# Kernel tuning notes

Hardware: AMD Instinct MI355X
Metric: run time of the kernel (lower is better)

The kernel has to match this reference:

```python
import jax, jax.numpy as jnp
import numpy as np

B, L, D = 4, 2048, 256
MAX_NGRAM = 3
SLOTS = 64


def setup_inputs() -> dict:
    key = jax.random.key(0)
    k1, k2, k3 = jax.random.split(key, 3)
    x = jax.random.normal(k1, (B, L, D), dtype=jnp.float32)
    memory = jax.random.normal(k2, (SLOTS, MAX_NGRAM, D), dtype=jnp.float32)
    pos_bias = jax.random.normal(k3, (SLOTS, MAX_NGRAM), dtype=jnp.float32)
    return {"x": x, "memory": memory, "pos_bias": pos_bias}


def _extract_ngrams(x, max_ngram):
    # Left-pad with max_ngram-1 zero vectors, then take max_ngram shifted views.
    b, l, d = x.shape
    xpad = jnp.concatenate([jnp.zeros((b, max_ngram - 1, d), x.dtype), x], axis=1)
    # ngrams[b, l, n] = xpad[b, n + l]  -> (B, L, N, d)
    return jnp.stack([xpad[:, n:n + l] for n in range(max_ngram)], axis=2)


def reference(x, memory, pos_bias):
    slots, max_ngram, d = memory.shape
    ngrams = _extract_ngrams(x, max_ngram)                      # (B, L, N, d)
    # Contraction over d replaces the huge (B,L,M,N,d) broadcast-multiply.
    sims = jnp.einsum('blnd,mnd->blmn', ngrams, memory)         # (B, L, M, N)
    scores = sims + pos_bias[None, None]                        # (B, L, M, N)
    best = jnp.argmax(scores, axis=-1)                          # (B, L, M) int
    # selected[b,l,m] = memory[m, best[b,l,m]]  -> (B, L, M, d)
    selected = memory[jnp.arange(slots)[None, None, :], best]
    return selected.sum(axis=2)                                 # (B, L, d)
```

## Files before the change

### kernel.cpp

```cpp
#include <hip/hip_runtime.h>
#include <stdint.h>

#define LL   2048
#define DD   256
#define SLOTS 64
#define MN   192
#define PT   8192

typedef _Float16 half8 __attribute__((ext_vector_type(8)));
typedef float    f32x4 __attribute__((ext_vector_type(4)));

#define FRAG_ELEMS (MN * DD)

__global__ __launch_bounds__(256) void prep_kernel(
    const float* __restrict__ mem,
    _Float16* __restrict__ aS_h, _Float16* __restrict__ aS_l,
    _Float16* __restrict__ bG_h)
{
    const int e = blockIdx.x * 256 + threadIdx.x;
    const int mnp = e >> 8;
    const int d   = e & 255;
    const int n = mnp >> 6, m = mnp & 63;
    const float v = mem[((m * 3 + n) << 8) + d];
    const _Float16 h  = (_Float16)v;
    const _Float16 lo = (_Float16)(v - (float)h);

    {
        const int tm = mnp >> 4, r = mnp & 15;
        const int c = d >> 5, q = (d >> 3) & 3, j = d & 7;
        const int i1 = ((tm * 8 + c) * 64 + (q * 16 + r)) * 8 + j;
        aS_h[i1] = h; aS_l[i1] = lo;
    }
    {
        const int c2 = mnp >> 5, q2 = (mnp >> 3) & 3, j2 = mnp & 7;
        const int td = d >> 4, n2 = d & 15;
        const int i2 = ((td * 6 + c2) * 64 + (q2 * 16 + n2)) * 8 + j2;
        bG_h[i2] = h;
    }
}

__global__ __launch_bounds__(768, 3) void fused_kernel(
    const float* __restrict__ x, const float* __restrict__ bias,
    const _Float16* __restrict__ aS_h, const _Float16* __restrict__ aS_l,
    const _Float16* __restrict__ bG_h,
    float* __restrict__ out)
{
    __shared__ __align__(16) _Float16 xfh[3 * 8 * 64 * 8];
    __shared__ __align__(16) _Float16 xfl[3 * 8 * 64 * 8];
    __shared__ float    scores[MN * 35];
    __shared__ float    biasS[MN];
    __shared__ uint32_t selS[32 * 8];

    const int p0   = blockIdx.x * 32;
    const int tid  = threadIdx.x;
    const int lane = tid & 63;
    const int w    = tid >> 6;
    const int q    = lane >> 4, col = lane & 15;
    const int tm   = w;

    half8 ah[2], al[2];
    {
        const size_t off = (size_t)((tm * 8 + 0) * 64 + lane) * 8;
        ah[0] = *(const half8*)(aS_h + off);
        al[0] = *(const half8*)(aS_l + off);
    }

    if (tid < MN) {
        const int m = tid & 63, n = tid >> 6;
        biasS[tid] = bias[m * 3 + n];
    }

#pragma unroll
    for (int k = 0; k < 2; ++k) {
        const int idx = tid + k * 768;
        const int rr  = idx >> 5;
        const int ch  = idx & 31;
        int g = p0 - 2 + rr;
        g = g < 0 ? 0 : (g > PT - 1 ? PT - 1 : g);
        const float4* xr = (const float4*)(x + (size_t)g * DD + ch * 8);
        const float4 u = xr[0];
        const float4 v = xr[1];
        float f[8] = {u.x, u.y, u.z, u.w, v.x, v.y, v.z, v.w};
        half8 hi, lo;
#pragma unroll
        for (int j = 0; j < 8; ++j) {
            const _Float16 hh = (_Float16)f[j];
            hi[j] = hh;
            lo[j] = (_Float16)(f[j] - (float)hh);
        }
        const int c = ch >> 2, qq = ch & 3;
        const int pt = rr >> 4, lr = rr & 15;
        const int base = ((pt * 8 + c) * 64 + qq * 16 + lr) * 8;
        *(half8*)(xfh + base) = hi;
        *(half8*)(xfl + base) = lo;
    }
    __syncthreads();

    {
        f32x4 acc[3];
#pragma unroll
        for (int p = 0; p < 3; ++p) acc[p] = (f32x4){0.f, 0.f, 0.f, 0.f};

        half8 bh[2][3], bl[2][3];
#pragma unroll
        for (int p = 0; p < 3; ++p) {
            const int base = ((p * 8 + 0) * 64 + lane) * 8;
            bh[0][p] = *(const half8*)(xfh + base);
            bl[0][p] = *(const half8*)(xfl + base);
        }

#pragma unroll
        for (int c = 0; c < 8; ++c) {
            const int cur = c & 1, nxt = cur ^ 1;
            if (c < 7) {
                const size_t off = (size_t)((tm * 8 + c + 1) * 64 + lane) * 8;
                ah[nxt] = *(const half8*)(aS_h + off);
                al[nxt] = *(const half8*)(aS_l + off);
#pragma unroll
                for (int p = 0; p < 3; ++p) {
                    const int base = ((p * 8 + c + 1) * 64 + lane) * 8;
                    bh[nxt][p] = *(const half8*)(xfh + base);
                    bl[nxt][p] = *(const half8*)(xfl + base);
                }
            }
#pragma unroll
            for (int p = 0; p < 3; ++p) {
                acc[p] = __builtin_amdgcn_mfma_f32_16x16x32_f16(ah[cur], bh[cur][p], acc[p], 0, 0, 0);
                acc[p] = __builtin_amdgcn_mfma_f32_16x16x32_f16(ah[cur], bl[cur][p], acc[p], 0, 0, 0);
                acc[p] = __builtin_amdgcn_mfma_f32_16x16x32_f16(al[cur], bh[cur][p], acc[p], 0, 0, 0);
            }
        }

#pragma unroll
        for (int p = 0; p < 3; ++p) {
            const int wp = p * 16 + col;
            if (wp < 34) {
#pragma unroll
                for (int r = 0; r < 4; ++r)
                    scores[(tm * 16 + q * 4 + r) * 35 + wp] = acc[p][r];
            }
        }
    }

    half8 mg[2];
    mg[0] = *(const half8*)(bG_h + (size_t)((w * 6 + 0) * 64 + lane) * 8);
    __syncthreads();

    for (int pl = w; pl < 32; pl += 12) {
        const int m = lane;
        const int p = p0 + pl;
        const int l = p & (LL - 1);
        const float v0 = ((l >= 2) ? scores[(      m) * 35 + pl + 0] : 0.f) + biasS[      m];
        const float v1 = ((l >= 1) ? scores[( 64 + m) * 35 + pl + 1] : 0.f) + biasS[ 64 + m];
        const float v2 =             scores[(128 + m) * 35 + pl + 2]        + biasS[128 + m];
        int bn = 0; float bv = v0;
        if (v1 > bv) { bv = v1; bn = 1; }
        if (v2 > bv) { bv = v2; bn = 2; }
        const unsigned long long b0 = __ballot(bn == 0);
        const unsigned long long b1 = __ballot(bn == 1);
        const unsigned long long b2 = __ballot(bn == 2);
        if (lane < 6) {
            const unsigned long long B = (lane >> 1) == 0 ? b0 : ((lane >> 1) == 1 ? b1 : b2);
            selS[pl * 8 + lane] = (uint32_t)(B >> ((lane & 1) * 32));
        }
    }
    __syncthreads();

    {
        const _Float16 ONE = (_Float16)1.f, ZERO = (_Float16)0.f;
        const int qb = q * 8;
#pragma unroll
        for (int ti = 0; ti < 3; ++ti) {
            const int t = w + ti * 12;
            if (t < 32) {
                const int pt = t >> 4, td = t & 15;
                uint32_t sw[6];
#pragma unroll
                for (int c = 0; c < 6; ++c) sw[c] = selS[(pt * 16 + col) * 8 + c];

                f32x4 acc2 = (f32x4){0.f, 0.f, 0.f, 0.f};
#pragma unroll
                for (int c = 0; c < 6; ++c) {
                    const int cur = c & 1, nxt = cur ^ 1;
                    if (c < 5) {
                        mg[nxt] = *(const half8*)(bG_h + (size_t)((td * 6 + c + 1) * 64 + lane) * 8);
                    } else {
                        const int tn = t + 12;
                        if (tn < 32) {
                            const int tdn = tn & 15;
                            mg[nxt] = *(const half8*)(bG_h + (size_t)((tdn * 6 + 0) * 64 + lane) * 8);
                        }
                    }
                    half8 sel;
#pragma unroll
                    for (int j = 0; j < 8; ++j)
                        sel[j] = ((sw[c] >> (qb + j)) & 1u) ? ONE : ZERO;
                    acc2 = __builtin_amdgcn_mfma_f32_16x16x32_f16(sel, mg[cur], acc2, 0, 0, 0);
                }

#pragma unroll
                for (int r = 0; r < 4; ++r)
                    out[(size_t)(p0 + pt * 16 + q * 4 + r) * DD + td * 16 + col] = acc2[r];
            }
        }
    }
}

extern "C" void kernel_launch(void* const* d_in, const int* in_sizes, int n_in,
                              void* d_out, int out_size, void* d_ws, size_t ws_size,
                              hipStream_t stream) {
    (void)in_sizes; (void)n_in; (void)out_size; (void)ws_size;
    const float* x    = (const float*)d_in[0];
    const float* mem  = (const float*)d_in[1];
    const float* bias = (const float*)d_in[2];
    float* out = (float*)d_out;

    _Float16* aS_h = (_Float16*)d_ws;
    _Float16* aS_l = aS_h + FRAG_ELEMS;
    _Float16* bG_h = aS_l + FRAG_ELEMS;

    prep_kernel<<<FRAG_ELEMS / 256, 256, 0, stream>>>(mem, aS_h, aS_l, bG_h);
    fused_kernel<<<PT / 32, 768, 0, stream>>>(x, bias, aS_h, aS_l, bG_h, out);
}
```

Measured before the change: 73.32 us.

## Fuse memory fp16 split prep into main kernel and stage gather operand in LDS

Removes the separate prep kernel. Each block now reads the fp32 memory table directly, splits it into hi/lo fp16 MFMA A-fragments held in registers, and writes the hi-only gather operand into shared memory. The x staging buffer is aliased with the score buffer to keep LDS usage in check. This drops one kernel launch and the workspace round trip, at the cost of every block redundantly converting the whole memory table, plus higher register and LDS pressure.

```diff
diff --git a/kernel.cpp b/kernel.cpp
--- a/kernel.cpp
+++ b/kernel.cpp
@@ -10,46 +10,19 @@
 typedef _Float16 half8 __attribute__((ext_vector_type(8)));
 typedef float    f32x4 __attribute__((ext_vector_type(4)));
 
-#define FRAG_ELEMS (MN * DD)
-
-__global__ __launch_bounds__(256) void prep_kernel(
-    const float* __restrict__ mem,
-    _Float16* __restrict__ aS_h, _Float16* __restrict__ aS_l,
-    _Float16* __restrict__ bG_h)
-{
-    const int e = blockIdx.x * 256 + threadIdx.x;
-    const int mnp = e >> 8;
-    const int d   = e & 255;
-    const int n = mnp >> 6, m = mnp & 63;
-    const float v = mem[((m * 3 + n) << 8) + d];
-    const _Float16 h  = (_Float16)v;
-    const _Float16 lo = (_Float16)(v - (float)h);
-
-    {
-        const int tm = mnp >> 4, r = mnp & 15;
-        const int c = d >> 5, q = (d >> 3) & 3, j = d & 7;
-        const int i1 = ((tm * 8 + c) * 64 + (q * 16 + r)) * 8 + j;
-        aS_h[i1] = h; aS_l[i1] = lo;
-    }
-    {
-        const int c2 = mnp >> 5, q2 = (mnp >> 3) & 3, j2 = mnp & 7;
-        const int td = d >> 4, n2 = d & 15;
-        const int i2 = ((td * 6 + c2) * 64 + (q2 * 16 + n2)) * 8 + j2;
-        bG_h[i2] = h;
-    }
-}
-
 __global__ __launch_bounds__(768, 3) void fused_kernel(
-    const float* __restrict__ x, const float* __restrict__ bias,
-    const _Float16* __restrict__ aS_h, const _Float16* __restrict__ aS_l,
-    const _Float16* __restrict__ bG_h,
+    const float* __restrict__ x, const float* __restrict__ mem,
+    const float* __restrict__ bias,
     float* __restrict__ out)
 {
-    __shared__ __align__(16) _Float16 xfh[3 * 8 * 64 * 8];
-    __shared__ __align__(16) _Float16 xfl[3 * 8 * 64 * 8];
-    __shared__ float    scores[MN * 35];
+    __shared__ __align__(16) char xbuf[49152];
+    __shared__ __align__(16) _Float16 bGs[16 * 6 * 64 * 8];
     __shared__ float    biasS[MN];
-    __shared__ uint32_t selS[32 * 8];
+    __shared__ uint32_t selS[32 * 6];
+
+    _Float16* xfh = (_Float16*)xbuf;
+    _Float16* xfl = (_Float16*)(xbuf + 24576);
+    float*    scores = (float*)xbuf;
 
     const int p0   = blockIdx.x * 32;
     const int tid  = threadIdx.x;
@@ -58,21 +31,28 @@
     const int q    = lane >> 4, col = lane & 15;
     const int tm   = w;
 
-    half8 ah[2], al[2];
-    {
-        const size_t off = (size_t)((tm * 8 + 0) * 64 + lane) * 8;
-        ah[0] = *(const half8*)(aS_h + off);
-        al[0] = *(const half8*)(aS_l + off);
-    }
-
     if (tid < MN) {
         const int m = tid & 63, n = tid >> 6;
         biasS[tid] = bias[m * 3 + n];
     }
 
-#pragma unroll
-    for (int k = 0; k < 2; ++k) {
-        const int idx = tid + k * 768;
+    float gv[8][8];
+#pragma unroll
+    for (int k = 0; k < 8; ++k) {
+        const int combo = w + k * 12;
+        const int td = combo / 6, c2 = combo - td * 6;
+        const int q2 = lane >> 4, n2 = lane & 15;
+#pragma unroll
+        for (int j = 0; j < 8; ++j) {
+            const int mnp = c2 * 32 + q2 * 8 + j;
+            const int n = mnp >> 6, m = mnp & 63;
+            gv[k][j] = mem[(size_t)(m * 3 + n) * DD + td * 16 + n2];
+        }
+    }
+
+#pragma unroll
+    for (int kk = 0; kk < 2; ++kk) {
+        const int idx = tid + kk * 768;
         const int rr  = idx >> 5;
         const int ch  = idx & 31;
         int g = p0 - 2 + rr;
@@ -94,13 +74,53 @@
         *(half8*)(xfh + base) = hi;
         *(half8*)(xfl + base) = lo;
     }
-    __syncthreads();
-
+
+#pragma unroll
+    for (int k = 0; k < 8; ++k) {
+        const int combo = w + k * 12;
+        const int td = combo / 6, c2 = combo - td * 6;
+        half8 hv;
+#pragma unroll
+        for (int j = 0; j < 8; ++j) hv[j] = (_Float16)gv[k][j];
+        *(half8*)(bGs + (size_t)((td * 6 + c2) * 64 + lane) * 8) = hv;
+    }
+
+    half8 ah[8], al[8];
     {
-        f32x4 acc[3];
-#pragma unroll
-        for (int p = 0; p < 3; ++p) acc[p] = (f32x4){0.f, 0.f, 0.f, 0.f};
-
+        const int r = lane & 15;
+        const int mnp = tm * 16 + r;
+        const int n = mnp >> 6, m = mnp & 63;
+        const float* rowp = mem + (size_t)(m * 3 + n) * DD;
+#pragma unroll
+        for (int half = 0; half < 2; ++half) {
+            float4 u[4], v[4];
+#pragma unroll
+            for (int ci = 0; ci < 4; ++ci) {
+                const int c = half * 4 + ci;
+                const float4* ap = (const float4*)(rowp + c * 32 + q * 8);
+                u[ci] = ap[0];
+                v[ci] = ap[1];
+            }
+#pragma unroll
+            for (int ci = 0; ci < 4; ++ci) {
+                const int c = half * 4 + ci;
+                float f[8] = {u[ci].x, u[ci].y, u[ci].z, u[ci].w,
+                              v[ci].x, v[ci].y, v[ci].z, v[ci].w};
+#pragma unroll
+                for (int j = 0; j < 8; ++j) {
+                    const _Float16 hh = (_Float16)f[j];
+                    ah[c][j] = hh;
+                    al[c][j] = (_Float16)(f[j] - (float)hh);
+                }
+            }
+        }
+    }
+    __syncthreads();
+
+    f32x4 acc[3];
+#pragma unroll
+    for (int p = 0; p < 3; ++p) acc[p] = (f32x4){0.f, 0.f, 0.f, 0.f};
+    {
         half8 bh[2][3], bl[2][3];
 #pragma unroll
         for (int p = 0; p < 3; ++p) {
@@ -113,9 +133,6 @@
         for (int c = 0; c < 8; ++c) {
             const int cur = c & 1, nxt = cur ^ 1;
             if (c < 7) {
-                const size_t off = (size_t)((tm * 8 + c + 1) * 64 + lane) * 8;
-                ah[nxt] = *(const half8*)(aS_h + off);
-                al[nxt] = *(const half8*)(aS_l + off);
 #pragma unroll
                 for (int p = 0; p < 3; ++p) {
                     const int base = ((p * 8 + c + 1) * 64 + lane) * 8;
@@ -125,25 +142,23 @@
             }
 #pragma unroll
             for (int p = 0; p < 3; ++p) {
-                acc[p] = __builtin_amdgcn_mfma_f32_16x16x32_f16(ah[cur], bh[cur][p], acc[p], 0, 0, 0);
-                acc[p] = __builtin_amdgcn_mfma_f32_16x16x32_f16(ah[cur], bl[cur][p], acc[p], 0, 0, 0);
-                acc[p] = __builtin_amdgcn_mfma_f32_16x16x32_f16(al[cur], bh[cur][p], acc[p], 0, 0, 0);
-            }
-        }
-
-#pragma unroll
-        for (int p = 0; p < 3; ++p) {
-            const int wp = p * 16 + col;
-            if (wp < 34) {
-#pragma unroll
-                for (int r = 0; r < 4; ++r)
-                    scores[(tm * 16 + q * 4 + r) * 35 + wp] = acc[p][r];
-            }
-        }
-    }
-
-    half8 mg[2];
-    mg[0] = *(const half8*)(bG_h + (size_t)((w * 6 + 0) * 64 + lane) * 8);
+                acc[p] = __builtin_amdgcn_mfma_f32_16x16x32_f16(ah[c], bh[cur][p], acc[p], 0, 0, 0);
+                acc[p] = __builtin_amdgcn_mfma_f32_16x16x32_f16(ah[c], bl[cur][p], acc[p], 0, 0, 0);
+                acc[p] = __builtin_amdgcn_mfma_f32_16x16x32_f16(al[c], bh[cur][p], acc[p], 0, 0, 0);
+            }
+        }
+    }
+    __syncthreads();
+
+#pragma unroll
+    for (int p = 0; p < 3; ++p) {
+        const int wp = p * 16 + col;
+        if (wp < 34) {
+#pragma unroll
+            for (int r = 0; r < 4; ++r)
+                scores[(tm * 16 + q * 4 + r) * 35 + wp] = acc[p][r];
+        }
+    }
     __syncthreads();
 
     for (int pl = w; pl < 32; pl += 12) {
@@ -161,7 +176,7 @@
         const unsigned long long b2 = __ballot(bn == 2);
         if (lane < 6) {
             const unsigned long long B = (lane >> 1) == 0 ? b0 : ((lane >> 1) == 1 ? b1 : b2);
-            selS[pl * 8 + lane] = (uint32_t)(B >> ((lane & 1) * 32));
+            selS[pl * 6 + lane] = (uint32_t)(B >> ((lane & 1) * 32));
         }
     }
     __syncthreads();
@@ -176,21 +191,16 @@
                 const int pt = t >> 4, td = t & 15;
                 uint32_t sw[6];
 #pragma unroll
-                for (int c = 0; c < 6; ++c) sw[c] = selS[(pt * 16 + col) * 8 + c];
+                for (int c = 0; c < 6; ++c) sw[c] = selS[(pt * 16 + col) * 6 + c];
 
                 f32x4 acc2 = (f32x4){0.f, 0.f, 0.f, 0.f};
+                half8 mg[2];
+                mg[0] = *(const half8*)(bGs + (size_t)((td * 6 + 0) * 64 + lane) * 8);
 #pragma unroll
                 for (int c = 0; c < 6; ++c) {
                     const int cur = c & 1, nxt = cur ^ 1;
-                    if (c < 5) {
-                        mg[nxt] = *(const half8*)(bG_h + (size_t)((td * 6 + c + 1) * 64 + lane) * 8);
-                    } else {
-                        const int tn = t + 12;
-                        if (tn < 32) {
-                            const int tdn = tn & 15;
-                            mg[nxt] = *(const half8*)(bG_h + (size_t)((tdn * 6 + 0) * 64 + lane) * 8);
-                        }
-                    }
+                    if (c < 5)
+                        mg[nxt] = *(const half8*)(bGs + (size_t)((td * 6 + c + 1) * 64 + lane) * 8);
                     half8 sel;
 #pragma unroll
                     for (int j = 0; j < 8; ++j)
@@ -209,16 +219,11 @@
 extern "C" void kernel_launch(void* const* d_in, const int* in_sizes, int n_in,
                               void* d_out, int out_size, void* d_ws, size_t ws_size,
                               hipStream_t stream) {
-    (void)in_sizes; (void)n_in; (void)out_size; (void)ws_size;
+    (void)in_sizes; (void)n_in; (void)out_size; (void)d_ws; (void)ws_size;
     const float* x    = (const float*)d_in[0];
     const float* mem  = (const float*)d_in[1];
     const float* bias = (const float*)d_in[2];
     float* out = (float*)d_out;
 
-    _Float16* aS_h = (_Float16*)d_ws;
-    _Float16* aS_l = aS_h + FRAG_ELEMS;
-    _Float16* bG_h = aS_l + FRAG_ELEMS;
-
-    prep_kernel<<<FRAG_ELEMS / 256, 256, 0, stream>>>(mem, aS_h, aS_l, bG_h);
-    fused_kernel<<<PT / 32, 768, 0, stream>>>(x, bias, aS_h, aS_l, bG_h, out);
+    fused_kernel<<<PT / 32, 768, 0, stream>>>(x, mem, bias, out);
 }
```

Measured after the change: 76.41 us. +4.2%, slower.

## Stage memory fragments in LDS and alias score buffer onto x tiles

Applied to the files above, without the earlier changes.

Each block now copies the full fp16 memory fragment array for the gather GEMM into shared memory up front, and the second MFMA stage reads it from LDS instead of global. To make room, the scores buffer is aliased onto the x hi/lo fragment storage, which needs an extra barrier. Redundant x row loads beyond the 34 needed rows are skipped. LDS use grows to roughly 147KB per block, limiting residency to one block per CU.

```diff
diff --git a/kernel.cpp b/kernel.cpp
--- a/kernel.cpp
+++ b/kernel.cpp
@@ -45,11 +45,14 @@
     const _Float16* __restrict__ bG_h,
     float* __restrict__ out)
 {
-    __shared__ __align__(16) _Float16 xfh[3 * 8 * 64 * 8];
-    __shared__ __align__(16) _Float16 xfl[3 * 8 * 64 * 8];
-    __shared__ float    scores[MN * 35];
+    __shared__ __align__(16) char xbuf[49152];
+    __shared__ __align__(16) _Float16 bGs[16 * 6 * 64 * 8];
     __shared__ float    biasS[MN];
-    __shared__ uint32_t selS[32 * 8];
+    __shared__ uint32_t selS[32 * 6];
+
+    _Float16* xfh = (_Float16*)xbuf;
+    _Float16* xfl = (_Float16*)(xbuf + 24576);
+    float*    scores = (float*)xbuf;
 
     const int p0   = blockIdx.x * 32;
     const int tid  = threadIdx.x;
@@ -70,37 +73,46 @@
         biasS[tid] = bias[m * 3 + n];
     }
 
-#pragma unroll
-    for (int k = 0; k < 2; ++k) {
-        const int idx = tid + k * 768;
-        const int rr  = idx >> 5;
-        const int ch  = idx & 31;
-        int g = p0 - 2 + rr;
-        g = g < 0 ? 0 : (g > PT - 1 ? PT - 1 : g);
-        const float4* xr = (const float4*)(x + (size_t)g * DD + ch * 8);
-        const float4 u = xr[0];
-        const float4 v = xr[1];
-        float f[8] = {u.x, u.y, u.z, u.w, v.x, v.y, v.z, v.w};
-        half8 hi, lo;
-#pragma unroll
-        for (int j = 0; j < 8; ++j) {
-            const _Float16 hh = (_Float16)f[j];
-            hi[j] = hh;
-            lo[j] = (_Float16)(f[j] - (float)hh);
-        }
-        const int c = ch >> 2, qq = ch & 3;
-        const int pt = rr >> 4, lr = rr & 15;
-        const int base = ((pt * 8 + c) * 64 + qq * 16 + lr) * 8;
-        *(half8*)(xfh + base) = hi;
-        *(half8*)(xfl + base) = lo;
-    }
-    __syncthreads();
-
-    {
-        f32x4 acc[3];
-#pragma unroll
-        for (int p = 0; p < 3; ++p) acc[p] = (f32x4){0.f, 0.f, 0.f, 0.f};
-
+    {
+        const half8* src = (const half8*)bG_h;
+        half8*       dst = (half8*)bGs;
+#pragma unroll
+        for (int i = 0; i < 8; ++i)
+            dst[tid + i * 768] = src[tid + i * 768];
+    }
+
+#pragma unroll
+    for (int kk = 0; kk < 2; ++kk) {
+        const int idx = tid + kk * 768;
+        if (idx < 1088) {
+            const int rr  = idx >> 5;
+            const int ch  = idx & 31;
+            int g = p0 - 2 + rr;
+            g = g < 0 ? 0 : g;
+            const float4* xr = (const float4*)(x + (size_t)g * DD + ch * 8);
+            const float4 u = xr[0];
+            const float4 v = xr[1];
+            float f[8] = {u.x, u.y, u.z, u.w, v.x, v.y, v.z, v.w};
+            half8 hi, lo;
+#pragma unroll
+            for (int j = 0; j < 8; ++j) {
+                const _Float16 hh = (_Float16)f[j];
+                hi[j] = hh;
+                lo[j] = (_Float16)(f[j] - (float)hh);
+            }
+            const int c = ch >> 2, qq = ch & 3;
+            const int pt = rr >> 4, lr = rr & 15;
+            const int base = ((pt * 8 + c) * 64 + qq * 16 + lr) * 8;
+            *(half8*)(xfh + base) = hi;
+            *(half8*)(xfl + base) = lo;
+        }
+    }
+    __syncthreads();
+
+    f32x4 acc[3];
+#pragma unroll
+    for (int p = 0; p < 3; ++p) acc[p] = (f32x4){0.f, 0.f, 0.f, 0.f};
+    {
         half8 bh[2][3], bl[2][3];
 #pragma unroll
         for (int p = 0; p < 3; ++p) {
@@ -130,20 +142,18 @@
                 acc[p] = __builtin_amdgcn_mfma_f32_16x16x32_f16(al[cur], bh[cur][p], acc[p], 0, 0, 0);
             }
         }
-
-#pragma unroll
-        for (int p = 0; p < 3; ++p) {
-            const int wp = p * 16 + col;
-            if (wp < 34) {
-#pragma unroll
-                for (int r = 0; r < 4; ++r)
-                    scores[(tm * 16 + q * 4 + r) * 35 + wp] = acc[p][r];
-            }
-        }
-    }
-
-    half8 mg[2];
-    mg[0] = *(const half8*)(bG_h + (size_t)((w * 6 + 0) * 64 + lane) * 8);
+    }
+    __syncthreads();
+
+#pragma unroll
+    for (int p = 0; p < 3; ++p) {
+        const int wp = p * 16 + col;
+        if (wp < 34) {
+#pragma unroll
+            for (int r = 0; r < 4; ++r)
+                scores[(tm * 16 + q * 4 + r) * 35 + wp] = acc[p][r];
+        }
+    }
     __syncthreads();
 
     for (int pl = w; pl < 32; pl += 12) {
@@ -161,7 +171,7 @@
         const unsigned long long b2 = __ballot(bn == 2);
         if (lane < 6) {
             const unsigned long long B = (lane >> 1) == 0 ? b0 : ((lane >> 1) == 1 ? b1 : b2);
-            selS[pl * 8 + lane] = (uint32_t)(B >> ((lane & 1) * 32));
+            selS[pl * 6 + lane] = (uint32_t)(B >> ((lane & 1) * 32));
         }
     }
     __syncthreads();
@@ -176,21 +186,16 @@
                 const int pt = t >> 4, td = t & 15;
                 uint32_t sw[6];
 #pragma unroll
-                for (int c = 0; c < 6; ++c) sw[c] = selS[(pt * 16 + col) * 8 + c];
+                for (int c = 0; c < 6; ++c) sw[c] = selS[(pt * 16 + col) * 6 + c];
 
                 f32x4 acc2 = (f32x4){0.f, 0.f, 0.f, 0.f};
+                half8 mg[2];
+                mg[0] = *(const half8*)(bGs + (size_t)((td * 6 + 0) * 64 + lane) * 8);
 #pragma unroll
                 for (int c = 0; c < 6; ++c) {
                     const int cur = c & 1, nxt = cur ^ 1;
-                    if (c < 5) {
-                        mg[nxt] = *(const half8*)(bG_h + (size_t)((td * 6 + c + 1) * 64 + lane) * 8);
-                    } else {
-                        const int tn = t + 12;
-                        if (tn < 32) {
-                            const int tdn = tn & 15;
-                            mg[nxt] = *(const half8*)(bG_h + (size_t)((tdn * 6 + 0) * 64 + lane) * 8);
-                        }
-                    }
+                    if (c < 5)
+                        mg[nxt] = *(const half8*)(bGs + (size_t)((td * 6 + c + 1) * 64 + lane) * 8);
                     half8 sel;
 #pragma unroll
                     for (int j = 0; j < 8; ++j)
```

After: 72.36 us. No clear change (-1.3%).
